# Optimization experiments

Measured on AMD Instinct MI355X. Metric: run time of the kernel, lower is better.

The kernel has to match this reference:

```python
import jax, jax.numpy as jnp
import numpy as np

N = 8192
IN_F = 512
OUT_F = 128
NEG_BIG = -9.0e15


def setup_inputs() -> dict:
    key = jax.random.key(0)
    k_x, k_adj, k_w, k_a1, k_a2 = jax.random.split(key, 5)
    X = jax.random.normal(k_x, (N, IN_F), dtype=jnp.float32)
    adj = jax.random.randint(k_adj, (N, N), 0, 2, dtype=jnp.int32)
    # xavier_uniform with gain=1.414
    gain = 1.414
    lim_w = gain * np.sqrt(6.0 / (IN_F + OUT_F))
    W = jax.random.uniform(k_w, (IN_F, OUT_F), minval=-lim_w, maxval=lim_w, dtype=jnp.float32)
    lim_a = gain * np.sqrt(6.0 / (OUT_F + 1))
    a_1 = jax.random.uniform(k_a1, (OUT_F, 1), minval=-lim_a, maxval=lim_a, dtype=jnp.float32)
    a_2 = jax.random.uniform(k_a2, (OUT_F, 1), minval=-lim_a, maxval=lim_a, dtype=jnp.float32)
    return {"X": X, "adj": adj, "W": W, "a_1": a_1, "a_2": a_2}


def reference(X, adj, W, a_1, a_2):
    h = X @ W                         # [N, out]
    Wh1 = h @ a_1                     # [N, 1]
    Wh2 = h @ a_2                     # [N, 1]
    alpha = Wh1 + Wh2.T               # [N, N] broadcast score sum
    s = jax.nn.sigmoid(alpha)
    masked = jnp.where(adj > 0, s, jnp.float32(NEG_BIG))
    attn = jax.nn.softmax(masked, axis=1)  # dropout p=0.0 -> identity
    return attn @ h                   # [N, out]
```

## Files before the change

kernel.cpp:

```cpp
#include <hip/hip_runtime.h>
#include <hip/hip_bf16.h>

#define N_NODES 8192
#define IN_F 512
#define OUT_F 128
#define NWAVE 16
#define KT_PER (256 / NWAVE)
#define LOG2E 1.4426950408889634f

typedef unsigned short u16;
typedef unsigned int u32;
typedef short s16x8 __attribute__((ext_vector_type(8)));
typedef float f32x4 __attribute__((ext_vector_type(4)));
typedef u32 u32x4 __attribute__((ext_vector_type(4)));

__device__ __forceinline__ u16 f2bf(float f) {
    union { float f; unsigned u; } x; x.f = f;
    unsigned r = x.u + 0x7FFFu + ((x.u >> 16) & 1u);
    return (u16)(r >> 16);
}

__device__ __forceinline__ u32 packbf2(float a, float b) {
    __hip_bfloat162 h = __float22bfloat162_rn(make_float2(a, b));
    u32 u; __builtin_memcpy(&u, &h, 4);
    return u;
}

__device__ __forceinline__ float edge_p(float wh1, float w2, int keep) {
    float alpha = wh1 + w2;
    float e = exp2f(-LOG2E * alpha);
    float s = __builtin_amdgcn_rcpf(1.0f + e);
    float p = exp2f(LOG2E * s);
    return keep ? p : 0.0f;
}

__global__ void repack_W(const float* __restrict__ W, u16* __restrict__ W_frag) {
    int tid = blockIdx.x * 256 + threadIdx.x;
    int j = tid & 7;
    int lane = (tid >> 3) & 63;
    int nt = (tid >> 9) & 7;
    int kt = tid >> 12;
    int k = kt * 32 + (lane >> 4) * 8 + j;
    int n = nt * 16 + (lane & 15);
    W_frag[tid] = f2bf(W[k * OUT_F + n]);
}

__global__ void compute_Wa(const float* __restrict__ W, const float* __restrict__ a1,
                           const float* __restrict__ a2,
                           float* __restrict__ Wa1, float* __restrict__ Wa2) {
    int k = blockIdx.x * 256 + threadIdx.x;
    if (k >= IN_F) return;
    float s1 = 0.f, s2 = 0.f;
    #pragma unroll 8
    for (int n = 0; n < OUT_F; n++) {
        float w = W[k * OUT_F + n];
        s1 += w * a1[n];
        s2 += w * a2[n];
    }
    Wa1[k] = s1; Wa2[k] = s2;
}

__global__ __launch_bounds__(256)
void gemm_h(const float* __restrict__ X, const u16* __restrict__ W_frag,
            const float* __restrict__ Wa1, const float* __restrict__ Wa2,
            float* __restrict__ Wh1, float* __restrict__ Wh2,
            u16* __restrict__ h_frag) {
    int tid = threadIdx.x;
    int wave = tid >> 6;
    int lane = tid & 63;
    int quad = lane >> 4;
    int lid = lane & 15;
    int rbase = blockIdx.x * 16;
    const float* xrow = X + (size_t)(rbase + lid) * IN_F;
    const s16x8* Wf = (const s16x8*)W_frag;
    f32x4 acc0 = {}, acc1 = {};
    float p1 = 0.f, p2 = 0.f;
    int nt0 = wave * 2;

    for (int kt = 0; kt < 16; kt++) {
        int k0 = kt * 32 + quad * 8;
        float4 x0 = *(const float4*)(xrow + k0);
        float4 x1 = *(const float4*)(xrow + k0 + 4);
        u32x4 uv;
        uv.x = packbf2(x0.x, x0.y); uv.y = packbf2(x0.z, x0.w);
        uv.z = packbf2(x1.x, x1.y); uv.w = packbf2(x1.z, x1.w);
        s16x8 a = __builtin_bit_cast(s16x8, uv);
        if (wave == 0) {
            float4 wa = *(const float4*)(Wa1 + k0);
            float4 wb = *(const float4*)(Wa1 + k0 + 4);
            float4 wc = *(const float4*)(Wa2 + k0);
            float4 wd = *(const float4*)(Wa2 + k0 + 4);
            p1 += x0.x*wa.x + x0.y*wa.y + x0.z*wa.z + x0.w*wa.w
                + x1.x*wb.x + x1.y*wb.y + x1.z*wb.z + x1.w*wb.w;
            p2 += x0.x*wc.x + x0.y*wc.y + x0.z*wc.z + x0.w*wc.w
                + x1.x*wd.x + x1.y*wd.y + x1.z*wd.z + x1.w*wd.w;
        }
        s16x8 b0 = Wf[(kt * 8 + nt0) * 64 + lane];
        s16x8 b1 = Wf[(kt * 8 + nt0 + 1) * 64 + lane];
        acc0 = __builtin_amdgcn_mfma_f32_16x16x32_bf16(a, b0, acc0, 0, 0, 0);
        acc1 = __builtin_amdgcn_mfma_f32_16x16x32_bf16(a, b1, acc1, 0, 0, 0);
    }

    #pragma unroll
    for (int reg = 0; reg < 4; reg++) {
        int row = rbase + quad * 4 + reg;
        int ktile = row >> 5, kl = row & 31;
        int lane2 = (kl >> 3) * 16 + lid, j2 = kl & 7;
        h_frag[(size_t)((ktile * 8 + nt0) * 64 + lane2) * 8 + j2] = f2bf(acc0[reg]);
        h_frag[(size_t)((ktile * 8 + nt0 + 1) * 64 + lane2) * 8 + j2] = f2bf(acc1[reg]);
    }
    if (wave == 0) {
        p1 += __shfl_xor(p1, 16, 64); p1 += __shfl_xor(p1, 32, 64);
        p2 += __shfl_xor(p2, 16, 64); p2 += __shfl_xor(p2, 32, 64);
        if (lane < 16) { Wh1[rbase + lid] = p1; Wh2[rbase + lid] = p2; }
    }
}

__global__ __launch_bounds__(1024, 4)
void attn_fused(const int* __restrict__ adj, const float* __restrict__ Wh1,
                const float* __restrict__ Wh2, const u16* __restrict__ h_frag,
                float* __restrict__ out) {
    __shared__ f32x4 red[8][16][64];
    __shared__ float rsum_lds[NWAVE][32];

    int tid = threadIdx.x;
    int wave = tid >> 6;
    int lane = tid & 63;
    int quad = lane >> 4;
    int lid = lane & 15;
    int rbase = blockIdx.x * 32;
    int r0 = rbase + lid, r1 = r0 + 16;

    float wh10 = Wh1[r0], wh11 = Wh1[r1];
    f32x4 acc0[8] = {}, acc1[8] = {};
    float ps0 = 0.f, ps1 = 0.f;
    const s16x8* Hf = (const s16x8*)h_frag;
    const int* adjrow0 = adj + (size_t)r0 * N_NODES;
    const int* adjrow1 = adj + (size_t)r1 * N_NODES;

    const int kt0 = wave * KT_PER;
    const int ktend = kt0 + KT_PER;

    int kpf = kt0 * 32 + quad * 8;
    int4 A0a = *(const int4*)(adjrow0 + kpf);
    int4 A0b = *(const int4*)(adjrow0 + kpf + 4);
    int4 A1a = *(const int4*)(adjrow1 + kpf);
    int4 A1b = *(const int4*)(adjrow1 + kpf + 4);

    #pragma unroll 1
    for (int kt = kt0; kt < ktend; kt++) {
        int k0 = kt * 32 + quad * 8;
        int4 aj0a = A0a, aj0b = A0b, aj1a = A1a, aj1b = A1b;
        int ktn = (kt + 1 < ktend) ? (kt + 1) : kt;
        int k0n = ktn * 32 + quad * 8;
        A0a = *(const int4*)(adjrow0 + k0n);
        A0b = *(const int4*)(adjrow0 + k0n + 4);
        A1a = *(const int4*)(adjrow1 + k0n);
        A1b = *(const int4*)(adjrow1 + k0n + 4);

        float4 w20 = *(const float4*)(Wh2 + k0);
        float4 w21 = *(const float4*)(Wh2 + k0 + 4);

        float e0 = edge_p(wh10, w20.x, aj0a.x), e1 = edge_p(wh10, w20.y, aj0a.y);
        float e2 = edge_p(wh10, w20.z, aj0a.z), e3 = edge_p(wh10, w20.w, aj0a.w);
        float e4 = edge_p(wh10, w21.x, aj0b.x), e5 = edge_p(wh10, w21.y, aj0b.y);
        float e6 = edge_p(wh10, w21.z, aj0b.z), e7 = edge_p(wh10, w21.w, aj0b.w);
        ps0 += ((e0 + e1) + (e2 + e3)) + ((e4 + e5) + (e6 + e7));
        u32x4 uv0;
        uv0.x = packbf2(e0, e1); uv0.y = packbf2(e2, e3);
        uv0.z = packbf2(e4, e5); uv0.w = packbf2(e6, e7);

        float f0 = edge_p(wh11, w20.x, aj1a.x), f1 = edge_p(wh11, w20.y, aj1a.y);
        float f2 = edge_p(wh11, w20.z, aj1a.z), f3 = edge_p(wh11, w20.w, aj1a.w);
        float f4 = edge_p(wh11, w21.x, aj1b.x), f5 = edge_p(wh11, w21.y, aj1b.y);
        float f6 = edge_p(wh11, w21.z, aj1b.z), f7 = edge_p(wh11, w21.w, aj1b.w);
        ps1 += ((f0 + f1) + (f2 + f3)) + ((f4 + f5) + (f6 + f7));
        u32x4 uv1;
        uv1.x = packbf2(f0, f1); uv1.y = packbf2(f2, f3);
        uv1.z = packbf2(f4, f5); uv1.w = packbf2(f6, f7);

        s16x8 af0 = __builtin_bit_cast(s16x8, uv0);
        s16x8 af1 = __builtin_bit_cast(s16x8, uv1);

        #pragma unroll
        for (int nt = 0; nt < 8; nt++) {
            s16x8 b = Hf[(kt * 8 + nt) * 64 + lane];
            acc0[nt] = __builtin_amdgcn_mfma_f32_16x16x32_bf16(af0, b, acc0[nt], 0, 0, 0);
            acc1[nt] = __builtin_amdgcn_mfma_f32_16x16x32_bf16(af1, b, acc1[nt], 0, 0, 0);
        }
    }

    ps0 += __shfl_xor(ps0, 16, 64); ps0 += __shfl_xor(ps0, 32, 64);
    ps1 += __shfl_xor(ps1, 16, 64); ps1 += __shfl_xor(ps1, 32, 64);
    if (lane < 16) {
        rsum_lds[wave][lane] = ps0;
        rsum_lds[wave][lane + 16] = ps1;
    }

    #pragma unroll
    for (int s = 8; s >= 1; s >>= 1) {
        if (wave >= s && wave < 2 * s) {
            #pragma unroll
            for (int nt = 0; nt < 8; nt++) {
                red[wave - s][nt][lane] = acc0[nt];
                red[wave - s][nt + 8][lane] = acc1[nt];
            }
        }
        __syncthreads();
        if (wave < s) {
            #pragma unroll
            for (int nt = 0; nt < 8; nt++) {
                acc0[nt] += red[wave][nt][lane];
                acc1[nt] += red[wave][nt + 8][lane];
            }
        }
        __syncthreads();
    }

    if (wave == 0) {
        #pragma unroll
        for (int reg = 0; reg < 4; reg++) {
            int row = quad * 4 + reg;
            float slo = 0.f, shi = 0.f;
            #pragma unroll
            for (int w = 0; w < NWAVE; w++) {
                slo += rsum_lds[w][row];
                shi += rsum_lds[w][row + 16];
            }
            float rlo = __builtin_amdgcn_rcpf(slo);
            float rhi = __builtin_amdgcn_rcpf(shi);
            rlo = rlo * (2.0f - slo * rlo);
            rhi = rhi * (2.0f - shi * rhi);
            #pragma unroll
            for (int nt = 0; nt < 8; nt++) {
                out[(size_t)(rbase + row) * OUT_F + nt * 16 + lid] = acc0[nt][reg] * rlo;
                out[(size_t)(rbase + row + 16) * OUT_F + nt * 16 + lid] = acc1[nt][reg] * rhi;
            }
        }
    }
}

extern "C" void kernel_launch(void* const* d_in, const int* in_sizes, int n_in,
                              void* d_out, int out_size, void* d_ws, size_t ws_size,
                              hipStream_t stream) {
    const float* X   = (const float*)d_in[0];
    const int*   adj = (const int*)d_in[1];
    const float* W   = (const float*)d_in[2];
    const float* a1  = (const float*)d_in[3];
    const float* a2  = (const float*)d_in[4];

    char* ws = (char*)d_ws;
    float* Wh1 = (float*)(ws);
    float* Wh2 = (float*)(ws + (32 << 10));
    float* Wa1 = (float*)(ws + (64 << 10));
    float* Wa2 = (float*)(ws + (66 << 10));
    u16* W_frag = (u16*)(ws + (128 << 10));
    u16* h_frag = (u16*)(ws + (256 << 10));
    float* out = (float*)d_out;

    hipLaunchKernelGGL(repack_W, dim3(256), dim3(256), 0, stream, W, W_frag);
    hipLaunchKernelGGL(compute_Wa, dim3(2), dim3(256), 0, stream, W, a1, a2, Wa1, Wa2);
    hipLaunchKernelGGL(gemm_h, dim3(512), dim3(256), 0, stream,
                       X, W_frag, Wa1, Wa2, Wh1, Wh2, h_frag);
    hipLaunchKernelGGL(attn_fused, dim3(N_NODES / 32), dim3(1024), 0, stream,
                       adj, Wh1, Wh2, h_frag, out);
}
```

Measured before the change: 459.6 us.

## Split row halves across waves, stagger k-tile start, flatten cross-wave reduction

Each wave now handles 16 rows over 32 k-tiles instead of 32 rows over 16 k-tiles. Waves are paired by row half across 8 k-stripes, which halves the accumulator registers per wave. Each block starts its k-loop at a rotated phase so blocks read different h_frag and adj regions at the same time. The tree reduction with many barriers is replaced by one LDS write, one barrier and a parallel sum where every wave writes one output tile. The trade-off is that each h_frag fragment is loaded twice per block, once for each row half, and the Wh2 prefetch adds register pressure.

```diff
diff --git a/kernel.cpp b/kernel.cpp
--- a/kernel.cpp
+++ b/kernel.cpp
@@ -4,8 +4,8 @@
 #define N_NODES 8192
 #define IN_F 512
 #define OUT_F 128
-#define NWAVE 16
-#define KT_PER (256 / NWAVE)
+#define NSTRIPE 8
+#define KT_PER 32
 #define LOG2E 1.4426950408889634f
 
 typedef unsigned short u16;
@@ -120,46 +120,46 @@
 void attn_fused(const int* __restrict__ adj, const float* __restrict__ Wh1,
                 const float* __restrict__ Wh2, const u16* __restrict__ h_frag,
                 float* __restrict__ out) {
-    __shared__ f32x4 red[8][16][64];
-    __shared__ float rsum_lds[NWAVE][32];
+    __shared__ f32x4 red[16][8][64];
+    __shared__ float rsum_lds[NSTRIPE][32];
 
     int tid = threadIdx.x;
     int wave = tid >> 6;
     int lane = tid & 63;
     int quad = lane >> 4;
     int lid = lane & 15;
+    int p = wave >> 1;
+    int h = wave & 1;
     int rbase = blockIdx.x * 32;
-    int r0 = rbase + lid, r1 = r0 + 16;
-
-    float wh10 = Wh1[r0], wh11 = Wh1[r1];
-    f32x4 acc0[8] = {}, acc1[8] = {};
-    float ps0 = 0.f, ps1 = 0.f;
+    int r0 = rbase + h * 16 + lid;
+
+    float wh10 = Wh1[r0];
+    f32x4 acc[8] = {};
+    float ps0 = 0.f;
     const s16x8* Hf = (const s16x8*)h_frag;
     const int* adjrow0 = adj + (size_t)r0 * N_NODES;
-    const int* adjrow1 = adj + (size_t)r1 * N_NODES;
-
-    const int kt0 = wave * KT_PER;
-    const int ktend = kt0 + KT_PER;
-
-    int kpf = kt0 * 32 + quad * 8;
+
+    const int kt0 = p * KT_PER;
+    const int phase = (blockIdx.x * 11) & (KT_PER - 1);
+
+    int ktc = kt0 + phase;
+    int kpf = ktc * 32 + quad * 8;
     int4 A0a = *(const int4*)(adjrow0 + kpf);
     int4 A0b = *(const int4*)(adjrow0 + kpf + 4);
-    int4 A1a = *(const int4*)(adjrow1 + kpf);
-    int4 A1b = *(const int4*)(adjrow1 + kpf + 4);
+    float4 W2a = *(const float4*)(Wh2 + kpf);
+    float4 W2b = *(const float4*)(Wh2 + kpf + 4);
 
     #pragma unroll 1
-    for (int kt = kt0; kt < ktend; kt++) {
-        int k0 = kt * 32 + quad * 8;
-        int4 aj0a = A0a, aj0b = A0b, aj1a = A1a, aj1b = A1b;
-        int ktn = (kt + 1 < ktend) ? (kt + 1) : kt;
+    for (int i = 0; i < KT_PER; i++) {
+        int kt = kt0 + ((i + phase) & (KT_PER - 1));
+        int4 aj0a = A0a, aj0b = A0b;
+        float4 w20 = W2a, w21 = W2b;
+        int ktn = kt0 + ((i + 1 + phase) & (KT_PER - 1));
         int k0n = ktn * 32 + quad * 8;
         A0a = *(const int4*)(adjrow0 + k0n);
         A0b = *(const int4*)(adjrow0 + k0n + 4);
-        A1a = *(const int4*)(adjrow1 + k0n);
-        A1b = *(const int4*)(adjrow1 + k0n + 4);
-
-        float4 w20 = *(const float4*)(Wh2 + k0);
-        float4 w21 = *(const float4*)(Wh2 + k0 + 4);
+        W2a = *(const float4*)(Wh2 + k0n);
+        W2b = *(const float4*)(Wh2 + k0n + 4);
 
         float e0 = edge_p(wh10, w20.x, aj0a.x), e1 = edge_p(wh10, w20.y, aj0a.y);
         float e2 = edge_p(wh10, w20.z, aj0a.z), e3 = edge_p(wh10, w20.w, aj0a.w);
@@ -169,74 +169,36 @@
         u32x4 uv0;
         uv0.x = packbf2(e0, e1); uv0.y = packbf2(e2, e3);
         uv0.z = packbf2(e4, e5); uv0.w = packbf2(e6, e7);
-
-        float f0 = edge_p(wh11, w20.x, aj1a.x), f1 = edge_p(wh11, w20.y, aj1a.y);
-        float f2 = edge_p(wh11, w20.z, aj1a.z), f3 = edge_p(wh11, w20.w, aj1a.w);
-        float f4 = edge_p(wh11, w21.x, aj1b.x), f5 = edge_p(wh11, w21.y, aj1b.y);
-        float f6 = edge_p(wh11, w21.z, aj1b.z), f7 = edge_p(wh11, w21.w, aj1b.w);
-        ps1 += ((f0 + f1) + (f2 + f3)) + ((f4 + f5) + (f6 + f7));
-        u32x4 uv1;
-        uv1.x = packbf2(f0, f1); uv1.y = packbf2(f2, f3);
-        uv1.z = packbf2(f4, f5); uv1.w = packbf2(f6, f7);
-
         s16x8 af0 = __builtin_bit_cast(s16x8, uv0);
-        s16x8 af1 = __builtin_bit_cast(s16x8, uv1);
 
         #pragma unroll
         for (int nt = 0; nt < 8; nt++) {
             s16x8 b = Hf[(kt * 8 + nt) * 64 + lane];
-            acc0[nt] = __builtin_amdgcn_mfma_f32_16x16x32_bf16(af0, b, acc0[nt], 0, 0, 0);
-            acc1[nt] = __builtin_amdgcn_mfma_f32_16x16x32_bf16(af1, b, acc1[nt], 0, 0, 0);
+            acc[nt] = __builtin_amdgcn_mfma_f32_16x16x32_bf16(af0, b, acc[nt], 0, 0, 0);
         }
     }
 
     ps0 += __shfl_xor(ps0, 16, 64); ps0 += __shfl_xor(ps0, 32, 64);
-    ps1 += __shfl_xor(ps1, 16, 64); ps1 += __shfl_xor(ps1, 32, 64);
-    if (lane < 16) {
-        rsum_lds[wave][lane] = ps0;
-        rsum_lds[wave][lane + 16] = ps1;
-    }
-
-    #pragma unroll
-    for (int s = 8; s >= 1; s >>= 1) {
-        if (wave >= s && wave < 2 * s) {
-            #pragma unroll
-            for (int nt = 0; nt < 8; nt++) {
-                red[wave - s][nt][lane] = acc0[nt];
-                red[wave - s][nt + 8][lane] = acc1[nt];
-            }
-        }
-        __syncthreads();
-        if (wave < s) {
-            #pragma unroll
-            for (int nt = 0; nt < 8; nt++) {
-                acc0[nt] += red[wave][nt][lane];
-                acc1[nt] += red[wave][nt + 8][lane];
-            }
-        }
-        __syncthreads();
-    }
-
-    if (wave == 0) {
+    if (lane < 16) rsum_lds[p][h * 16 + lane] = ps0;
+
+    #pragma unroll
+    for (int nt = 0; nt < 8; nt++) red[wave][nt][lane] = acc[nt];
+    __syncthreads();
+
+    int h2 = wave & 1, nt2 = wave >> 1;
+    f32x4 s = red[h2][nt2][lane];
+    #pragma unroll
+    for (int p2 = 1; p2 < NSTRIPE; p2++) s += red[p2 * 2 + h2][nt2][lane];
+
+    #pragma unroll
+    for (int reg = 0; reg < 4; reg++) {
+        int rowl = quad * 4 + reg;
+        float sum = 0.f;
         #pragma unroll
-        for (int reg = 0; reg < 4; reg++) {
-            int row = quad * 4 + reg;
-            float slo = 0.f, shi = 0.f;
-            #pragma unroll
-            for (int w = 0; w < NWAVE; w++) {
-                slo += rsum_lds[w][row];
-                shi += rsum_lds[w][row + 16];
-            }
-            float rlo = __builtin_amdgcn_rcpf(slo);
-            float rhi = __builtin_amdgcn_rcpf(shi);
-            rlo = rlo * (2.0f - slo * rlo);
-            rhi = rhi * (2.0f - shi * rhi);
-            #pragma unroll
-            for (int nt = 0; nt < 8; nt++) {
-                out[(size_t)(rbase + row) * OUT_F + nt * 16 + lid] = acc0[nt][reg] * rlo;
-                out[(size_t)(rbase + row + 16) * OUT_F + nt * 16 + lid] = acc1[nt][reg] * rhi;
-            }
-        }
+        for (int p2 = 0; p2 < NSTRIPE; p2++) sum += rsum_lds[p2][h2 * 16 + rowl];
+        float r = __builtin_amdgcn_rcpf(sum);
+        r = r * (2.0f - sum * r);
+        out[(size_t)(rbase + h2 * 16 + rowl) * OUT_F + nt2 * 16 + lid] = s[reg] * r;
     }
 }
 
```

Result: faster. 430.7 us (-6.3%).

## Pack adjacency into bitmask and use 8 K-stripes with parallel reduction

Applied to the files above, without the earlier changes.

Adds a pre-pass that compresses the int32 adjacency matrix into a 32-bit-per-word bitmask. The attention kernel then reads bits instead of int4 vectors. The attention kernel drops from 16 waves to 8 waves per block, each covering twice as many K-tiles, and replaces the serial tree reduction with a single LDS exchange where every wave reduces and writes one column tile. The full 256MB adj read still happens in the pack kernel, so the gain depends on the pack pass streaming more efficiently than the fused kernel's int reads. It also cuts reduction syncs.

```diff
diff --git a/kernel.cpp b/kernel.cpp
--- a/kernel.cpp
+++ b/kernel.cpp
@@ -4,8 +4,9 @@
 #define N_NODES 8192
 #define IN_F 512
 #define OUT_F 128
-#define NWAVE 16
-#define KT_PER (256 / NWAVE)
+#define NSTRIPE 8
+#define KT_PER 32
+#define NWORDS (N_NODES / 32)
 #define LOG2E 1.4426950408889634f
 
 typedef unsigned short u16;
@@ -58,6 +59,22 @@
         s2 += w * a2[n];
     }
     Wa1[k] = s1; Wa2[k] = s2;
+}
+
+__global__ __launch_bounds__(256)
+void pack_adj(const int* __restrict__ adj, u32* __restrict__ Pk) {
+    int gid = blockIdx.x * 256 + threadIdx.x;
+    const int* src = adj + (size_t)gid * 32;
+    u32 b = 0;
+    #pragma unroll
+    for (int t = 0; t < 8; t++) {
+        int4 v = *(const int4*)(src + t * 4);
+        b |= (u32)(v.x > 0) << (t * 4 + 0);
+        b |= (u32)(v.y > 0) << (t * 4 + 1);
+        b |= (u32)(v.z > 0) << (t * 4 + 2);
+        b |= (u32)(v.w > 0) << (t * 4 + 3);
+    }
+    Pk[gid] = b;
 }
 
 __global__ __launch_bounds__(256)
@@ -116,12 +133,12 @@
     }
 }
 
-__global__ __launch_bounds__(1024, 4)
-void attn_fused(const int* __restrict__ adj, const float* __restrict__ Wh1,
+__global__ __launch_bounds__(512)
+void attn_fused(const u32* __restrict__ Pk, const float* __restrict__ Wh1,
                 const float* __restrict__ Wh2, const u16* __restrict__ h_frag,
                 float* __restrict__ out) {
-    __shared__ f32x4 red[8][16][64];
-    __shared__ float rsum_lds[NWAVE][32];
+    __shared__ f32x4 red[NSTRIPE][16][64];
+    __shared__ float rsum_lds[NSTRIPE][32];
 
     int tid = threadIdx.x;
     int wave = tid >> 6;
@@ -135,58 +152,65 @@
     f32x4 acc0[8] = {}, acc1[8] = {};
     float ps0 = 0.f, ps1 = 0.f;
     const s16x8* Hf = (const s16x8*)h_frag;
-    const int* adjrow0 = adj + (size_t)r0 * N_NODES;
-    const int* adjrow1 = adj + (size_t)r1 * N_NODES;
+    const u32* prow0 = Pk + (size_t)r0 * NWORDS;
+    const u32* prow1 = Pk + (size_t)r1 * NWORDS;
 
     const int kt0 = wave * KT_PER;
-    const int ktend = kt0 + KT_PER;
-
-    int kpf = kt0 * 32 + quad * 8;
-    int4 A0a = *(const int4*)(adjrow0 + kpf);
-    int4 A0b = *(const int4*)(adjrow0 + kpf + 4);
-    int4 A1a = *(const int4*)(adjrow1 + kpf);
-    int4 A1b = *(const int4*)(adjrow1 + kpf + 4);
+
+    u32x4 P0 = *(const u32x4*)(prow0 + kt0);
+    u32x4 P1 = *(const u32x4*)(prow1 + kt0);
 
     #pragma unroll 1
-    for (int kt = kt0; kt < ktend; kt++) {
-        int k0 = kt * 32 + quad * 8;
-        int4 aj0a = A0a, aj0b = A0b, aj1a = A1a, aj1b = A1b;
-        int ktn = (kt + 1 < ktend) ? (kt + 1) : kt;
-        int k0n = ktn * 32 + quad * 8;
-        A0a = *(const int4*)(adjrow0 + k0n);
-        A0b = *(const int4*)(adjrow0 + k0n + 4);
-        A1a = *(const int4*)(adjrow1 + k0n);
-        A1b = *(const int4*)(adjrow1 + k0n + 4);
-
-        float4 w20 = *(const float4*)(Wh2 + k0);
-        float4 w21 = *(const float4*)(Wh2 + k0 + 4);
-
-        float e0 = edge_p(wh10, w20.x, aj0a.x), e1 = edge_p(wh10, w20.y, aj0a.y);
-        float e2 = edge_p(wh10, w20.z, aj0a.z), e3 = edge_p(wh10, w20.w, aj0a.w);
-        float e4 = edge_p(wh10, w21.x, aj0b.x), e5 = edge_p(wh10, w21.y, aj0b.y);
-        float e6 = edge_p(wh10, w21.z, aj0b.z), e7 = edge_p(wh10, w21.w, aj0b.w);
-        ps0 += ((e0 + e1) + (e2 + e3)) + ((e4 + e5) + (e6 + e7));
-        u32x4 uv0;
-        uv0.x = packbf2(e0, e1); uv0.y = packbf2(e2, e3);
-        uv0.z = packbf2(e4, e5); uv0.w = packbf2(e6, e7);
-
-        float f0 = edge_p(wh11, w20.x, aj1a.x), f1 = edge_p(wh11, w20.y, aj1a.y);
-        float f2 = edge_p(wh11, w20.z, aj1a.z), f3 = edge_p(wh11, w20.w, aj1a.w);
-        float f4 = edge_p(wh11, w21.x, aj1b.x), f5 = edge_p(wh11, w21.y, aj1b.y);
-        float f6 = edge_p(wh11, w21.z, aj1b.z), f7 = edge_p(wh11, w21.w, aj1b.w);
-        ps1 += ((f0 + f1) + (f2 + f3)) + ((f4 + f5) + (f6 + f7));
-        u32x4 uv1;
-        uv1.x = packbf2(f0, f1); uv1.y = packbf2(f2, f3);
-        uv1.z = packbf2(f4, f5); uv1.w = packbf2(f6, f7);
-
-        s16x8 af0 = __builtin_bit_cast(s16x8, uv0);
-        s16x8 af1 = __builtin_bit_cast(s16x8, uv1);
+    for (int g = 0; g < KT_PER / 4; g++) {
+        u32x4 c0 = P0, c1 = P1;
+        int gn = (g + 1 < KT_PER / 4) ? g + 1 : g;
+        P0 = *(const u32x4*)(prow0 + kt0 + gn * 4);
+        P1 = *(const u32x4*)(prow1 + kt0 + gn * 4);
 
         #pragma unroll
-        for (int nt = 0; nt < 8; nt++) {
-            s16x8 b = Hf[(kt * 8 + nt) * 64 + lane];
-            acc0[nt] = __builtin_amdgcn_mfma_f32_16x16x32_bf16(af0, b, acc0[nt], 0, 0, 0);
-            acc1[nt] = __builtin_amdgcn_mfma_f32_16x16x32_bf16(af1, b, acc1[nt], 0, 0, 0);
+        for (int t = 0; t < 4; t++) {
+            int kt = kt0 + g * 4 + t;
+            int k0 = kt * 32 + quad * 8;
+            u32 w0 = c0[t] >> (quad * 8);
+            u32 w1 = c1[t] >> (quad * 8);
+            float4 w20 = *(const float4*)(Wh2 + k0);
+            float4 w21 = *(const float4*)(Wh2 + k0 + 4);
+
+            float e0 = edge_p(wh10, w20.x, (w0 >> 0) & 1);
+            float e1 = edge_p(wh10, w20.y, (w0 >> 1) & 1);
+            float e2 = edge_p(wh10, w20.z, (w0 >> 2) & 1);
+            float e3 = edge_p(wh10, w20.w, (w0 >> 3) & 1);
+            float e4 = edge_p(wh10, w21.x, (w0 >> 4) & 1);
+            float e5 = edge_p(wh10, w21.y, (w0 >> 5) & 1);
+            float e6 = edge_p(wh10, w21.z, (w0 >> 6) & 1);
+            float e7 = edge_p(wh10, w21.w, (w0 >> 7) & 1);
+            ps0 += ((e0 + e1) + (e2 + e3)) + ((e4 + e5) + (e6 + e7));
+            u32x4 uv0;
+            uv0.x = packbf2(e0, e1); uv0.y = packbf2(e2, e3);
+            uv0.z = packbf2(e4, e5); uv0.w = packbf2(e6, e7);
+
+            float f0 = edge_p(wh11, w20.x, (w1 >> 0) & 1);
+            float f1 = edge_p(wh11, w20.y, (w1 >> 1) & 1);
+            float f2 = edge_p(wh11, w20.z, (w1 >> 2) & 1);
+            float f3 = edge_p(wh11, w20.w, (w1 >> 3) & 1);
+            float f4 = edge_p(wh11, w21.x, (w1 >> 4) & 1);
+            float f5 = edge_p(wh11, w21.y, (w1 >> 5) & 1);
+            float f6 = edge_p(wh11, w21.z, (w1 >> 6) & 1);
+            float f7 = edge_p(wh11, w21.w, (w1 >> 7) & 1);
+            ps1 += ((f0 + f1) + (f2 + f3)) + ((f4 + f5) + (f6 + f7));
+            u32x4 uv1;
+            uv1.x = packbf2(f0, f1); uv1.y = packbf2(f2, f3);
+            uv1.z = packbf2(f4, f5); uv1.w = packbf2(f6, f7);
+
+            s16x8 af0 = __builtin_bit_cast(s16x8, uv0);
+            s16x8 af1 = __builtin_bit_cast(s16x8, uv1);
+
+            #pragma unroll
+            for (int nt = 0; nt < 8; nt++) {
+                s16x8 b = Hf[(kt * 8 + nt) * 64 + lane];
+                acc0[nt] = __builtin_amdgcn_mfma_f32_16x16x32_bf16(af0, b, acc0[nt], 0, 0, 0);
+                acc1[nt] = __builtin_amdgcn_mfma_f32_16x16x32_bf16(af1, b, acc1[nt], 0, 0, 0);
+            }
         }
     }
 
@@ -198,44 +222,29 @@
     }
 
     #pragma unroll
-    for (int s = 8; s >= 1; s >>= 1) {
-        if (wave >= s && wave < 2 * s) {
-            #pragma unroll
-            for (int nt = 0; nt < 8; nt++) {
-                red[wave - s][nt][lane] = acc0[nt];
-                red[wave - s][nt + 8][lane] = acc1[nt];
-            }
-        }
-        __syncthreads();
-        if (wave < s) {
-            #pragma unroll
-            for (int nt = 0; nt < 8; nt++) {
-                acc0[nt] += red[wave][nt][lane];
-                acc1[nt] += red[wave][nt + 8][lane];
-            }
-        }
-        __syncthreads();
-    }
-
-    if (wave == 0) {
+    for (int nt = 0; nt < 8; nt++) {
+        red[wave][nt][lane] = acc0[nt];
+        red[wave][nt + 8][lane] = acc1[nt];
+    }
+    __syncthreads();
+
+    #pragma unroll
+    for (int half = 0; half < 2; half++) {
+        int i = wave + half * 8;
+        int rowoff = half * 16;
+        f32x4 s = red[0][i][lane];
+        #pragma unroll
+        for (int p2 = 1; p2 < NSTRIPE; p2++) s += red[p2][i][lane];
+
         #pragma unroll
         for (int reg = 0; reg < 4; reg++) {
-            int row = quad * 4 + reg;
-            float slo = 0.f, shi = 0.f;
+            int rowl = quad * 4 + reg;
+            float sum = 0.f;
             #pragma unroll
-            for (int w = 0; w < NWAVE; w++) {
-                slo += rsum_lds[w][row];
-                shi += rsum_lds[w][row + 16];
-            }
-            float rlo = __builtin_amdgcn_rcpf(slo);
-            float rhi = __builtin_amdgcn_rcpf(shi);
-            rlo = rlo * (2.0f - slo * rlo);
-            rhi = rhi * (2.0f - shi * rhi);
-            #pragma unroll
-            for (int nt = 0; nt < 8; nt++) {
-                out[(size_t)(rbase + row) * OUT_F + nt * 16 + lid] = acc0[nt][reg] * rlo;
-                out[(size_t)(rbase + row + 16) * OUT_F + nt * 16 + lid] = acc1[nt][reg] * rhi;
-            }
+            for (int p2 = 0; p2 < NSTRIPE; p2++) sum += rsum_lds[p2][rowoff + rowl];
+            float r = __builtin_amdgcn_rcpf(sum);
+            r = r * (2.0f - sum * r);
+            out[(size_t)(rbase + rowoff + rowl) * OUT_F + wave * 16 + lid] = s[reg] * r;
         }
     }
 }
@@ -256,12 +265,14 @@
     float* Wa2 = (float*)(ws + (66 << 10));
     u16* W_frag = (u16*)(ws + (128 << 10));
     u16* h_frag = (u16*)(ws + (256 << 10));
+    u32* Pk     = (u32*)(ws + ((size_t)4 << 20));
     float* out = (float*)d_out;
 
     hipLaunchKernelGGL(repack_W, dim3(256), dim3(256), 0, stream, W, W_frag);
     hipLaunchKernelGGL(compute_Wa, dim3(2), dim3(256), 0, stream, W, a1, a2, Wa1, Wa2);
+    hipLaunchKernelGGL(pack_adj, dim3(N_NODES * NWORDS / 256), dim3(256), 0, stream, adj, Pk);
     hipLaunchKernelGGL(gemm_h, dim3(512), dim3(256), 0, stream,
                        X, W_frag, Wa1, Wa2, Wh1, Wh2, h_frag);
-    hipLaunchKernelGGL(attn_fused, dim3(N_NODES / 32), dim3(1024), 0, stream,
-                       adj, Wh1, Wh2, h_frag, out);
-}
+    hipLaunchKernelGGL(attn_fused, dim3(N_NODES / 32), dim3(512), 0, stream,
+                       Pk, Wh1, Wh2, h_frag, out);
+}
```

New measurement: 469.2 us. 2.1% more time.
